# Kernel optimization log

Measured on AMD Instinct MI355X. Metric: run time of the kernel, lower is better.

## Reference

```python
import jax, jax.numpy as jnp
import numpy as np

H = 256; NH = 8; DH = H // NH; L = 2; B = 32; S = 512; FIN = 199; A = 4


def _ln(x, g, b):
    m = jnp.mean(x, -1, keepdims=True)
    v = jnp.mean((x - m) ** 2, -1, keepdims=True)
    return (x - m) / jnp.sqrt(v + 1e-5) * g + b


def _grn(x, fc1w, fc1b, fc2w, fc2b, gw, gb, ggw, ggb, lg, lb):
    # GatedResidualNetwork, input_dim == output_dim so no skip layer, no context
    h = jax.nn.elu(x @ fc1w + fc1b)
    h = jax.nn.elu(h @ fc2w + fc2b)
    g = (h @ gw + gb) * jax.nn.sigmoid(h @ ggw + ggb)  # GLU
    return _ln(g + x, lg, lb)


def _attn(h, wq, bq, wk, bk, wv, bv, wo, bo):
    b, s, _ = h.shape
    q = (h @ wq + bq).reshape(b, s, NH, DH)
    k = (h @ wk + bk).reshape(b, s, NH, DH)
    v = (h @ wv + bv).reshape(b, s, NH, DH)
    scores = jnp.einsum('bqhd,bkhd->bhqk', q, k) / jnp.sqrt(jnp.float32(DH))
    mask = jnp.triu(jnp.ones((s, s), dtype=bool), 1)  # causal: mask strictly-future
    scores = jnp.where(mask, -jnp.inf, scores)
    aw = jax.nn.softmax(scores, axis=-1)
    ctx = jnp.einsum('bhqk,bkhd->bqhd', aw, v).reshape(b, s, H)
    return ctx @ wo + bo, aw


def _pe(s, d):
    pos = jnp.arange(s, dtype=jnp.float32)[:, None]
    div = jnp.exp(jnp.arange(0, d, 2, dtype=jnp.float32) * (-jnp.log(10000.0) / d))
    pe = jnp.zeros((s, d), dtype=jnp.float32)
    pe = pe.at[:, 0::2].set(jnp.sin(pos * div)).at[:, 1::2].set(jnp.cos(pos * div))
    return pe


def setup_inputs():
    key = jax.random.key(0)
    ks = iter(jax.random.split(key, 80))
    def nrm(shape, sc=0.02):
        return (jax.random.normal(next(ks), shape) * sc).astype(jnp.float32)
    d = {}
    d['x'] = jax.random.normal(next(ks), (B, S, FIN), dtype=jnp.float32)
    d['time_features'] = jax.random.normal(next(ks), (B, S, 3), dtype=jnp.float32)
    d['fp_w'] = nrm((FIN, H)); d['fp_b'] = jnp.zeros((H,), jnp.float32)
    d['tp_w'] = nrm((3, H));   d['tp_b'] = jnp.zeros((H,), jnp.float32)
    d['ip_w'] = nrm((H, H));   d['ip_b'] = jnp.zeros((H,), jnp.float32)
    for nm in ['wq', 'wk', 'wv', 'wo']:
        d[nm] = nrm((L, H, H))
    for nm in ['bq', 'bk', 'bv', 'bo']:
        d[nm] = jnp.zeros((L, H), jnp.float32)
    d['ln_g'] = jnp.ones((L, H), jnp.float32); d['ln_b'] = jnp.zeros((L, H), jnp.float32)
    for nm in ['g_fc1w', 'g_fc2w', 'g_gw', 'g_ggw']:
        d[nm] = nrm((L, H, H))
    for nm in ['g_fc1b', 'g_fc2b', 'g_gb', 'g_ggb']:
        d[nm] = jnp.zeros((L, H), jnp.float32)
    d['g_lg'] = jnp.ones((L, H), jnp.float32); d['g_lb'] = jnp.zeros((L, H), jnp.float32)
    for nm in ['f_fc1w', 'f_fc2w', 'f_gw', 'f_ggw']:
        d[nm] = nrm((H, H))
    for nm in ['f_fc1b', 'f_fc2b', 'f_gb', 'f_ggb']:
        d[nm] = jnp.zeros((H,), jnp.float32)
    d['f_lg'] = jnp.ones((H,), jnp.float32); d['f_lb'] = jnp.zeros((H,), jnp.float32)
    d['out_w'] = nrm((H, A)); d['out_b'] = jnp.zeros((A,), jnp.float32)
    return d


def reference(x, time_features, fp_w, fp_b, tp_w, tp_b, ip_w, ip_b,
              wq, bq, wk, bk, wv, bv, wo, bo, ln_g, ln_b,
              g_fc1w, g_fc1b, g_fc2w, g_fc2b, g_gw, g_gb, g_ggw, g_ggb, g_lg, g_lb,
              f_fc1w, f_fc1b, f_fc2w, f_fc2b, f_gw, f_gb, f_ggw, f_ggb, f_lg, f_lb,
              out_w, out_b):
    s = x.shape[1]
    hidden = (x @ fp_w + fp_b) + (time_features @ tp_w + tp_b)
    hidden = hidden @ ip_w + ip_b
    hidden = hidden + _pe(s, H)[None]
    aw = None
    for i in range(L):
        ao, aw = _attn(hidden, wq[i], bq[i], wk[i], bk[i], wv[i], bv[i], wo[i], bo[i])
        hidden = _ln(hidden + ao, ln_g[i], ln_b[i])
        hidden = _grn(hidden, g_fc1w[i], g_fc1b[i], g_fc2w[i], g_fc2b[i],
                      g_gw[i], g_gb[i], g_ggw[i], g_ggb[i], g_lg[i], g_lb[i])
    hidden = _grn(hidden, f_fc1w, f_fc1b, f_fc2w, f_fc2b, f_gw, f_gb, f_ggw, f_ggb, f_lg, f_lb)
    final = hidden[:, -1, :]
    logits = final @ out_w + out_b  # [B, A], one column per target asset
    return (logits, aw)
```

## Files before the change

kernel.cpp:

```cpp
#include <hip/hip_runtime.h>
#include <hip/hip_fp16.h>
#include <math.h>
#include <cstddef>

#define H 256
#define NH 8
#define DH 32
#define LAYERS 2
#define BB 32
#define SS 512
#define FINDIM 199
#define AA 4
#define T_TOK (BB*SS)
#define KIN 224
#define TPB 64

typedef unsigned short u16;
typedef unsigned int u32;
typedef __attribute__((ext_vector_type(8))) short short8;
typedef __attribute__((ext_vector_type(4))) float f4;

__device__ __forceinline__ float b2f(u16 v){
  unsigned u = ((unsigned)v) << 16;
  return __builtin_bit_cast(float, u);
}
__device__ __forceinline__ u16 f2b(float f){
  unsigned u = __builtin_bit_cast(unsigned, f);
  unsigned r = (u + 0x7fffu + ((u >> 16) & 1u)) >> 16;
  return (u16)r;
}
__device__ __forceinline__ float wave_sum(float v){
  #pragma unroll
  for (int mk=1; mk<64; mk<<=1) v += __shfl_xor(v, mk, 64);
  return v;
}

#define GLD_LDS16(g, l) \
  __builtin_amdgcn_global_load_lds((const __attribute__((address_space(1))) void*)(g), \
                                   (__attribute__((address_space(3))) void*)(l), 16, 0, 0)

#define SA (KIN+8)
#define SY (H+8)

template<int KC, int WK>
__device__ __forceinline__ void stage_acc64(
    const u16* Xl, int sx, const u16* __restrict__ Wt,
    int r0, int c0, int l16, int lq, f4 acc[2][4])
{
  #pragma unroll
  for (int mi=0;mi<2;mi++)
    #pragma unroll
    for (int ni=0;ni<4;ni++) acc[mi][ni] = (f4){0.f,0.f,0.f,0.f};
  #pragma unroll
  for (int kc=0;kc<KC;kc++){
    short8 af[2], bf[4];
    #pragma unroll
    for (int mi=0;mi<2;mi++)
      af[mi] = *(const short8*)&Xl[(r0 + mi*16 + l16)*sx + kc*32 + lq*8];
    #pragma unroll
    for (int ni=0;ni<4;ni++)
      bf[ni] = *(const short8*)(Wt + (size_t)(c0 + ni*16 + l16)*WK + kc*32 + lq*8);
    #pragma unroll
    for (int mi=0;mi<2;mi++)
      #pragma unroll
      for (int ni=0;ni<4;ni++)
        acc[mi][ni] = __builtin_amdgcn_mfma_f32_16x16x32_bf16(af[mi], bf[ni], acc[mi][ni], 0,0,0);
  }
}

template<int DO_ELU>
__device__ __forceinline__ void stage_store64(
    f4 acc[2][4], const float* __restrict__ bias,
    int r0, int c0, int l16, int lq, u16* Yl, int sy)
{
  #pragma unroll
  for (int ni=0;ni<4;ni++){
    int col = c0 + ni*16 + l16;
    float bc = bias[col];
    #pragma unroll
    for (int mi=0;mi<2;mi++){
      #pragma unroll
      for (int r=0;r<4;r++){
        int row = r0 + mi*16 + lq*4 + r;
        float v = acc[mi][ni][r] + bc;
        if (DO_ELU) v = v > 0.f ? v : expm1f(v);
        Yl[row*sy + col] = f2b(v);
      }
    }
  }
}

__device__ __forceinline__ void tile_load64(const u16* g, u16* Yl, int sy, int t){
  #pragma unroll
  for (int j=0;j<4;j++){
    int u = t + j*512;
    int row = u >> 5, cu = u & 31;
    *(short8*)&Yl[row*sy + cu*8] = *(const short8*)(g + (size_t)row*H + cu*8);
  }
}

template<int WB>
__device__ __forceinline__ void tile_ln64(
    u16* Yl, int sy, const float* __restrict__ g, const float* __restrict__ b,
    u16* out, int t)
{
  int w = t >> 6, lane = t & 63;
  #pragma unroll
  for (int rr=0;rr<8;rr++){
    int row = w*8 + rr;
    float xv[4];
    #pragma unroll
    for (int j=0;j<4;j++) xv[j] = b2f(Yl[row*sy + lane*4 + j]);
    float s=0.f, ss=0.f;
    #pragma unroll
    for (int j=0;j<4;j++){ s += xv[j]; ss += xv[j]*xv[j]; }
    s = wave_sum(s); ss = wave_sum(ss);
    float mean = s * (1.0f/H);
    float var  = ss * (1.0f/H) - mean*mean;
    float rstd = rsqrtf(var + 1e-5f);
    ushort4 o;
    int col = lane*4;
    o.x = f2b((xv[0]-mean)*rstd*g[col+0] + b[col+0]);
    o.y = f2b((xv[1]-mean)*rstd*g[col+1] + b[col+1]);
    o.z = f2b((xv[2]-mean)*rstd*g[col+2] + b[col+2]);
    o.w = f2b((xv[3]-mean)*rstd*g[col+3] + b[col+3]);
    *(ushort4*)(out + (size_t)row*H + col) = o;
    if (WB && row == 63) *(ushort4*)(Yl + row*sy + col) = o;
  }
}

struct WPtrs { const float* p[21]; };

__global__ __launch_bounds__(256) void wconv_kernel(WPtrs wp, u16* __restrict__ dst){
  __shared__ float tl[64][65];
  int mb = blockIdx.x >> 4, tile = blockIdx.x & 15;
  int k0 = (tile >> 2) * 64, n0 = (tile & 3) * 64;
  const float* src = wp.p[mb];
  int t = threadIdx.x;
  int r = t >> 4, cg = t & 15;
  #pragma unroll
  for (int p4=0;p4<4;p4++){
    f4 v = *(const f4*)(src + (size_t)(k0 + r + p4*16)*H + n0 + cg*4);
    tl[r+p4*16][cg*4+0]=v[0]; tl[r+p4*16][cg*4+1]=v[1];
    tl[r+p4*16][cg*4+2]=v[2]; tl[r+p4*16][cg*4+3]=v[3];
  }
  __syncthreads();
  u16* db = dst + (size_t)mb*H*H;
  #pragma unroll
  for (int p4=0;p4<4;p4++){
    int rn = r + p4*16;
    ushort4 o;
    o.x = f2b(tl[cg*4+0][rn]); o.y = f2b(tl[cg*4+1][rn]);
    o.z = f2b(tl[cg*4+2][rn]); o.w = f2b(tl[cg*4+3][rn]);
    *(ushort4*)(db + (size_t)(n0+rn)*H + k0 + cg*4) = o;
  }
}

__global__ __launch_bounds__(256) void wcat_kernel(
    const float* __restrict__ fp_w, const float* __restrict__ tp_w,
    u16* __restrict__ wcat){
  int idx = blockIdx.x*256 + threadIdx.x;
  if (idx >= 256*KIN) return;
  int n = idx / KIN, k2 = idx % KIN;
  float v = 0.f;
  if (k2 < FINDIM) v = fp_w[(size_t)k2*H + n];
  else if (k2 < FINDIM+3) v = tp_w[(size_t)(k2-FINDIM)*H + n];
  wcat[idx] = f2b(v);
}

__global__ __launch_bounds__(256) void xconv_kernel(
    const float* __restrict__ x, const float* __restrict__ tf,
    u16* __restrict__ ab){
  size_t idx = (size_t)blockIdx.x*256 + threadIdx.x;
  if (idx >= (size_t)T_TOK*KIN) return;
  int tok = idx / KIN, k2 = idx % KIN;
  float v = 0.f;
  if (k2 < FINDIM) v = x[(size_t)tok*FINDIM + k2];
  else if (k2 < FINDIM+3) v = tf[(size_t)tok*3 + (k2-FINDIM)];
  ab[idx] = f2b(v);
}

__global__ __launch_bounds__(512,4) void input_kernel(
    const u16* __restrict__ ab, const u16* __restrict__ wcat,
    const float* __restrict__ fp_b, const float* __restrict__ tp_b,
    const u16* __restrict__ ipw, const float* __restrict__ ip_b,
    u16* __restrict__ hid){
  __shared__ u16 Al[TPB*SA];
  __shared__ u16 Tl[TPB*SY];
  int t = threadIdx.x;
  int tok0 = blockIdx.x * TPB;
  int lane = t & 63, w = t >> 6;
  int l16 = lane & 15, lq = lane >> 4;
  int r0 = (w >> 2) * 32;
  int c0 = (w & 3) * 64;

  #pragma unroll
  for (int j=0;j<4;j++){
    int u = t + j*512;
    if (u < 1792){
      int row = u / 28, cu = u % 28;
      *(short8*)&Al[row*SA + cu*8] = *(const short8*)(ab + (size_t)(tok0+row)*KIN + cu*8);
    }
  }
  __syncthreads();

  f4 acc[2][4];
  stage_acc64<7, KIN>(Al, SA, wcat, r0, c0, l16, lq, acc);
  #pragma unroll
  for (int ni=0;ni<4;ni++){
    int col = c0 + ni*16 + l16;
    float bc = fp_b[col] + tp_b[col];
    #pragma unroll
    for (int mi=0;mi<2;mi++)
      #pragma unroll
      for (int r=0;r<4;r++){
        int row = r0 + mi*16 + lq*4 + r;
        Tl[row*SY + col] = f2b(acc[mi][ni][r] + bc);
      }
  }
  __syncthreads();

  stage_acc64<8, H>(Tl, SY, ipw, r0, c0, l16, lq, acc);
  #pragma unroll
  for (int ni=0;ni<4;ni++){
    int col = c0 + ni*16 + l16;
    float bc = ip_b[col];
    int ii = col >> 1;
    float div = __expf((float)(2*ii) * -0.03597789207803197f);
    #pragma unroll
    for (int mi=0;mi<2;mi++)
      #pragma unroll
      for (int r=0;r<4;r++){
        int row = r0 + mi*16 + lq*4 + r;
        int s = (tok0 + row) & (SS-1);
        float arg = (float)s * div;
        float pe = (col & 1) ? cosf(arg) : sinf(arg);
        hid[(size_t)(tok0+row)*H + col] = f2b(acc[mi][ni][r] + bc + pe);
      }
  }
}

__global__ __launch_bounds__(512,4) void oproj_ln_kernel(
    const u16* __restrict__ ctx, u16* __restrict__ hid,
    const u16* __restrict__ wo, const float* __restrict__ bo,
    const float* __restrict__ g, const float* __restrict__ b){
  __shared__ u16 Xl[TPB*SY];
  int t = threadIdx.x;
  int tok0 = blockIdx.x * TPB;
  int lane = t & 63, w = t >> 6;
  int l16 = lane & 15, lq = lane >> 4;
  int r0 = (w >> 2) * 32;
  int c0 = (w & 3) * 64;
  u16* hb = hid + (size_t)tok0*H;

  tile_load64(ctx + (size_t)tok0*H, Xl, SY, t);
  __syncthreads();

  f4 acc[2][4];
  stage_acc64<8, H>(Xl, SY, wo, r0, c0, l16, lq, acc);
  __syncthreads();
  #pragma unroll
  for (int ni=0;ni<4;ni++){
    int col = c0 + ni*16 + l16;
    float bc = bo[col];
    #pragma unroll
    for (int mi=0;mi<2;mi++)
      #pragma unroll
      for (int r=0;r<4;r++){
        int row = r0 + mi*16 + lq*4 + r;
        float y = acc[mi][ni][r] + bc + b2f(hb[(size_t)row*H + col]);
        Xl[row*SY + col] = f2b(y);
      }
  }
  __syncthreads();
  tile_ln64<0>(Xl, SY, g, b, hb, t);
}

template<int LOGITS>
__global__ __launch_bounds__(512,4) void grn_kernel(
    u16* __restrict__ hid,
    const u16* __restrict__ fc1, const u16* __restrict__ fc2,
    const u16* __restrict__ gw,  const u16* __restrict__ ggw,
    const float* __restrict__ b1, const float* __restrict__ b2,
    const float* __restrict__ gb, const float* __restrict__ ggb,
    const float* __restrict__ lg, const float* __restrict__ lb,
    const float* __restrict__ ow, const float* __restrict__ ob,
    float* __restrict__ lout){
  __shared__ u16 Xa[TPB*SY];
  __shared__ u16 Xb[TPB*SY];
  int t = threadIdx.x;
  int tok0 = blockIdx.x * TPB;
  int lane = t & 63, w = t >> 6;
  int l16 = lane & 15, lq = lane >> 4;
  int r0 = (w >> 2) * 32;
  int c0 = (w & 3) * 64;
  u16* hb = hid + (size_t)tok0*H;

  tile_load64(hb, Xa, SY, t);
  __syncthreads();

  f4 acc[2][4];
  stage_acc64<8, H>(Xa, SY, fc1, r0, c0, l16, lq, acc);
  stage_store64<1>(acc, b1, r0, c0, l16, lq, Xb, SY);
  __syncthreads();
  stage_acc64<8, H>(Xb, SY, fc2, r0, c0, l16, lq, acc);
  stage_store64<1>(acc, b2, r0, c0, l16, lq, Xa, SY);
  __syncthreads();

  stage_acc64<8, H>(Xa, SY, ggw, r0, c0, l16, lq, acc);
  u32 sgp[2][4][2];
  #pragma unroll
  for (int mi=0;mi<2;mi++)
    #pragma unroll
    for (int ni=0;ni<4;ni++){
      float bc = ggb[c0 + ni*16 + l16];
      float s0 = 1.0f/(1.0f + __expf(-(acc[mi][ni][0]+bc)));
      float s1 = 1.0f/(1.0f + __expf(-(acc[mi][ni][1]+bc)));
      float s2 = 1.0f/(1.0f + __expf(-(acc[mi][ni][2]+bc)));
      float s3 = 1.0f/(1.0f + __expf(-(acc[mi][ni][3]+bc)));
      sgp[mi][ni][0] = __builtin_bit_cast(u32, __floats2half2_rn(s0, s1));
      sgp[mi][ni][1] = __builtin_bit_cast(u32, __floats2half2_rn(s2, s3));
    }

  stage_acc64<8, H>(Xa, SY, gw, r0, c0, l16, lq, acc);
  #pragma unroll
  for (int ni=0;ni<4;ni++){
    int col = c0 + ni*16 + l16;
    float bc = gb[col];
    #pragma unroll
    for (int mi=0;mi<2;mi++){
      float2 s01 = __half22float2(__builtin_bit_cast(__half2, sgp[mi][ni][0]));
      float2 s23 = __half22float2(__builtin_bit_cast(__half2, sgp[mi][ni][1]));
      float sv[4] = {s01.x, s01.y, s23.x, s23.y};
      #pragma unroll
      for (int r=0;r<4;r++){
        int row = r0 + mi*16 + lq*4 + r;
        float y = (acc[mi][ni][r] + bc) * sv[r] + b2f(hb[(size_t)row*H + col]);
        Xb[row*SY + col] = f2b(y);
      }
    }
  }
  __syncthreads();
  tile_ln64<LOGITS>(Xb, SY, lg, lb, hb, t);

  if (LOGITS){
    if ((tok0 & (SS-1)) == SS - TPB){
      __syncthreads();
      if (t < 64){
        int bidx = tok0 >> 9;
        float a0=0.f, a1=0.f, a2=0.f, a3=0.f;
        #pragma unroll
        for (int j=0;j<4;j++){
          int k = t*4 + j;
          float xv = b2f(Xb[63*SY + k]);
          f4 wr = *(const f4*)(ow + (size_t)k*AA);
          a0 = fmaf(xv, wr[0], a0);
          a1 = fmaf(xv, wr[1], a1);
          a2 = fmaf(xv, wr[2], a2);
          a3 = fmaf(xv, wr[3], a3);
        }
        a0 = wave_sum(a0); a1 = wave_sum(a1);
        a2 = wave_sum(a2); a3 = wave_sum(a3);
        if (t == 0){
          lout[bidx*AA+0] = a0 + ob[0];
          lout[bidx*AA+1] = a1 + ob[1];
          lout[bidx*AA+2] = a2 + ob[2];
          lout[bidx*AA+3] = a3 + ob[3];
        }
      }
    }
  }
}

struct GemmJob  { const u16* Wt; const float* bias; u16* C; };
struct GemmBatch{ GemmJob j[3]; };

__global__ __launch_bounds__(256) void gemm_bf16(
    const u16* __restrict__ A, GemmBatch jb) {
  __shared__ u16 smem[128*64 + 64*64];
  u16* As  = smem;
  u16* Wsm = smem + 128*64;
  const GemmJob job = jb.j[blockIdx.z];
  const u16* Wt = job.Wt;
  int t = threadIdx.x;
  int m0 = blockIdx.x * 128;
  int n0 = blockIdx.y * 64;
  int lane = t & 63, w = t >> 6;
  int wr = (w >> 1) * 64;
  int wc = (w & 1) * 32;
  int l16 = lane & 15, lq = lane >> 4;

  f4 acc[4][2];
  #pragma unroll
  for (int mi=0;mi<4;mi++)
    #pragma unroll
    for (int ni=0;ni<2;ni++) acc[mi][ni] = (f4){0.f,0.f,0.f,0.f};

  for (int k0=0;k0<256;k0+=64){
    #pragma unroll
    for (int ja=0;ja<4;ja++){
      int ub = (w*4 + ja)*64;
      int u  = ub + lane;
      int m  = u >> 3, c = u & 7, kx = c ^ (m & 7);
      const u16* g = A + (size_t)(m0+m)*H + k0 + kx*8;
      GLD_LDS16(g, As + (size_t)ub*8);
    }
    #pragma unroll
    for (int jb2=0;jb2<2;jb2++){
      int ub = (w*2 + jb2)*64;
      int u  = ub + lane;
      int n  = u >> 3, c = u & 7, kx = c ^ (n & 7);
      const u16* g = Wt + (size_t)(n0+n)*H + k0 + kx*8;
      GLD_LDS16(g, Wsm + (size_t)ub*8);
    }
    __syncthreads();
    #pragma unroll
    for (int kc=0;kc<2;kc++){
      short8 af[4], bf[2];
      int kx = kc*4 + lq;
      #pragma unroll
      for (int mi=0;mi<4;mi++){
        int m = wr + mi*16 + l16;
        int un = (m<<3) | (kx ^ (m&7));
        af[mi] = *(short8*)&As[un*8];
      }
      #pragma unroll
      for (int ni=0;ni<2;ni++){
        int n = wc + ni*16 + l16;
        int un = (n<<3) | (kx ^ (n&7));
        bf[ni] = *(short8*)&Wsm[un*8];
      }
      #pragma unroll
      for (int mi=0;mi<4;mi++)
        #pragma unroll
        for (int ni=0;ni<2;ni++)
          acc[mi][ni] = __builtin_amdgcn_mfma_f32_16x16x32_bf16(af[mi], bf[ni], acc[mi][ni], 0,0,0);
    }
    __syncthreads();
  }

  u16* Cl = smem;
  #pragma unroll
  for (int ni=0;ni<2;ni++){
    int coll = wc + ni*16 + l16;
    float bcol = job.bias[n0 + coll];
    #pragma unroll
    for (int mi=0;mi<4;mi++){
      #pragma unroll
      for (int r=0;r<4;r++){
        int rowl = wr + mi*16 + lq*4 + r;
        Cl[rowl*68 + coll] = f2b(acc[mi][ni][r] + bcol);
      }
    }
  }
  __syncthreads();
  #pragma unroll
  for (int q2=0;q2<4;q2++){
    int u = q2*256 + t;
    int row = u >> 3, cu = u & 7;
    short8 val = *(short8*)&Cl[row*68 + cu*8];
    *(short8*)(job.C + (size_t)(m0+row)*H + n0 + cu*8) = val;
  }
}

template<int WRITE_AW>
__global__ __launch_bounds__(256) void attn_kernel(
    const u16* __restrict__ q, const u16* __restrict__ k,
    const u16* __restrict__ v, float* __restrict__ aw,
    u16* __restrict__ ctx) {
  __shared__ u16 Vt[DH][SS+8];
  __shared__ u16 Plds[4][16][72];
  int t  = threadIdx.x;
  int zg = blockIdx.x;
  int bh = blockIdx.y;
  int b  = bh >> 3, h = bh & 7;
  int lane = t & 63, w = t >> 6;
  int l16 = lane & 15, lq = lane >> 4;
  const float scale = 0.17677669529663687f;

  #pragma unroll
  for (int rep=0;rep<2;rep++){
    int kk = t + rep*256;
    const u16* vp = v + ((size_t)(b*SS + kk))*H + h*DH;
    short8 r0 = *(const short8*)(vp);
    short8 r1 = *(const short8*)(vp+8);
    short8 r2 = *(const short8*)(vp+16);
    short8 r3 = *(const short8*)(vp+24);
    #pragma unroll
    for (int j=0;j<8;j++){
      Vt[j][kk]    = (u16)r0[j];
      Vt[8+j][kk]  = (u16)r1[j];
      Vt[16+j][kk] = (u16)r2[j];
      Vt[24+j][kk] = (u16)r3[j];
    }
  }
  __syncthreads();

  for (int it=0; it<4; it++){
    int qt  = zg + it*2;
    int qr0 = qt*64 + w*16;
    int KT  = qt*4 + w + 1;
    short8 af = *(const short8*)(q + ((size_t)(b*SS + qr0 + l16))*H + h*DH + lq*8);

    float l[4] = {0.f,0.f,0.f,0.f};
    f4 o[2] = {(f4){0.f,0.f,0.f,0.f}, (f4){0.f,0.f,0.f,0.f}};
    u32 pk0[32], pk1[32];

    #pragma unroll
    for (int c8=0;c8<8;c8++){
      if (c8*4 < KT){
        #pragma unroll
        for (int j=0;j<4;j++){
          int kt = c8*4 + j;
          float p[4] = {0.f,0.f,0.f,0.f};
          if (kt < KT){
            short8 bfr = *(const short8*)(k + ((size_t)(b*SS + kt*16 + l16))*H + h*DH + lq*8);
            f4 cc = (f4){0.f,0.f,0.f,0.f};
            cc = __builtin_amdgcn_mfma_f32_16x16x32_bf16(af, bfr, cc, 0,0,0);
            int col = kt*16 + l16;
            #pragma unroll
            for (int i=0;i<4;i++){
              int qi = qr0 + lq*4 + i;
              float sc = (col <= qi) ? cc[i]*scale : -3.0e38f;
              p[i] = __expf(sc);
              l[i] += p[i];
            }
          }
          u16 pb[4];
          #pragma unroll
          for (int i=0;i<4;i++) pb[i] = f2b(p[i]);
          if (WRITE_AW){
            pk0[kt] = (u32)pb[0] | ((u32)pb[1] << 16);
            pk1[kt] = (u32)pb[2] | ((u32)pb[3] << 16);
          }
          #pragma unroll
          for (int i=0;i<4;i++) Plds[w][lq*4+i][j*16+l16] = pb[i];
        }
        #pragma unroll
        for (int kc=0;kc<2;kc++){
          short8 pa = *(short8*)&Plds[w][l16][kc*32 + lq*8];
          #pragma unroll
          for (int dt=0;dt<2;dt++){
            short8 vb = *(const short8*)&Vt[dt*16 + l16][c8*64 + kc*32 + lq*8];
            o[dt] = __builtin_amdgcn_mfma_f32_16x16x32_bf16(pa, vb, o[dt], 0,0,0);
          }
        }
      }
    }

    #pragma unroll
    for (int i=0;i<4;i++){
      #pragma unroll
      for (int mk=1; mk<16; mk<<=1) l[i] += __shfl_xor(l[i], mk, 64);
    }
    float inv[4];
    #pragma unroll
    for (int i=0;i<4;i++) inv[i] = 1.0f / l[i];

    if (WRITE_AW){
      float* ab = aw + (size_t)bh*SS*SS;
      #pragma unroll
      for (int kt=0;kt<32;kt++){
        if (kt < KT){
          int col = kt*16 + l16;
          float pv[4] = { b2f((u16)pk0[kt]), b2f((u16)(pk0[kt]>>16)),
                          b2f((u16)pk1[kt]), b2f((u16)(pk1[kt]>>16)) };
          #pragma unroll
          for (int i=0;i<4;i++){
            int qi = qr0 + lq*4 + i;
            float val = (col <= qi) ? pv[i]*inv[i] : 0.f;
            __builtin_nontemporal_store(val, &ab[(size_t)qi*SS + col]);
          }
        }
      }
      int c4base = KT*4;
      f4 z = (f4){0.f,0.f,0.f,0.f};
      #pragma unroll
      for (int ri=0;ri<4;ri++){
        int row = qr0 + ri*4 + lq;
        for (int j=l16; j < 128 - c4base; j += 16)
          __builtin_nontemporal_store(z, (f4*)&ab[(size_t)row*SS + (size_t)(c4base+j)*4]);
      }
    }

    #pragma unroll
    for (int dt=0;dt<2;dt++){
      #pragma unroll
      for (int i=0;i<4;i++){
        int row = qr0 + lq*4 + i;
        ctx[((size_t)(b*SS + row))*H + h*DH + dt*16 + l16] = f2b(o[dt][i]*inv[i]);
      }
    }
  }
}

extern "C" void kernel_launch(void* const* d_in, const int* in_sizes, int n_in,
                              void* d_out, int out_size, void* d_ws, size_t ws_size,
                              hipStream_t stream){
  (void)in_sizes; (void)n_in; (void)out_size; (void)ws_size;
  const float* x      = (const float*)d_in[0];
  const float* tf     = (const float*)d_in[1];
  const float* fp_w   = (const float*)d_in[2];
  const float* fp_b   = (const float*)d_in[3];
  const float* tp_w   = (const float*)d_in[4];
  const float* tp_b   = (const float*)d_in[5];
  const float* ip_w   = (const float*)d_in[6];
  const float* ip_b   = (const float*)d_in[7];
  const float* wq     = (const float*)d_in[8];
  const float* wk     = (const float*)d_in[9];
  const float* wv     = (const float*)d_in[10];
  const float* wo     = (const float*)d_in[11];
  const float* bq     = (const float*)d_in[12];
  const float* bk     = (const float*)d_in[13];
  const float* bv     = (const float*)d_in[14];
  const float* bo     = (const float*)d_in[15];
  const float* ln_g   = (const float*)d_in[16];
  const float* ln_b   = (const float*)d_in[17];
  const float* g_fc1w = (const float*)d_in[18];
  const float* g_fc2w = (const float*)d_in[19];
  const float* g_gw   = (const float*)d_in[20];
  const float* g_ggw  = (const float*)d_in[21];
  const float* g_fc1b = (const float*)d_in[22];
  const float* g_fc2b = (const float*)d_in[23];
  const float* g_gb   = (const float*)d_in[24];
  const float* g_ggb  = (const float*)d_in[25];
  const float* g_lg   = (const float*)d_in[26];
  const float* g_lb   = (const float*)d_in[27];
  const float* f_fc1w = (const float*)d_in[28];
  const float* f_fc2w = (const float*)d_in[29];
  const float* f_gw   = (const float*)d_in[30];
  const float* f_ggw  = (const float*)d_in[31];
  const float* f_fc1b = (const float*)d_in[32];
  const float* f_fc2b = (const float*)d_in[33];
  const float* f_gb   = (const float*)d_in[34];
  const float* f_ggb  = (const float*)d_in[35];
  const float* f_lg   = (const float*)d_in[36];
  const float* f_lb   = (const float*)d_in[37];
  const float* out_w  = (const float*)d_in[38];
  const float* out_b  = (const float*)d_in[39];

  float* logits = (float*)d_out;
  float* aw     = logits + BB*AA;

  u16* wts = (u16*)d_ws;
  const size_t WMAT = (size_t)H*H;
  u16* wcat = wts  + 21*WMAT;
  u16* abuf = wcat + (size_t)H*KIN;
  u16* hid  = abuf + (size_t)T_TOK*KIN;
  size_t BUF = (size_t)T_TOK * H;
  u16* buf1 = hid  + BUF;
  u16* buf2 = buf1 + BUF;
  u16* buf3 = buf2 + BUF;

  WPtrs wp;
  wp.p[0]  = ip_w;
  wp.p[1]  = wq;        wp.p[2]  = wq + WMAT;
  wp.p[3]  = wk;        wp.p[4]  = wk + WMAT;
  wp.p[5]  = wv;        wp.p[6]  = wv + WMAT;
  wp.p[7]  = wo;        wp.p[8]  = wo + WMAT;
  wp.p[9]  = g_fc1w;    wp.p[10] = g_fc1w + WMAT;
  wp.p[11] = g_fc2w;    wp.p[12] = g_fc2w + WMAT;
  wp.p[13] = g_gw;      wp.p[14] = g_gw + WMAT;
  wp.p[15] = g_ggw;     wp.p[16] = g_ggw + WMAT;
  wp.p[17] = f_fc1w;    wp.p[18] = f_fc2w;
  wp.p[19] = f_gw;      wp.p[20] = f_ggw;
  const int WT_IP=0, WT_Q=1, WT_K=3, WT_V=5, WT_O=7,
            WT_FC1=9, WT_FC2=11, WT_GW=13, WT_GGW=15,
            WT_FFC1=17, WT_FFC2=18, WT_FGW=19, WT_FGGW=20;

  dim3 b256(256), b512(512);
  dim3 gAttn(2, BB*NH);
  dim3 gTok(T_TOK/TPB);

  wconv_kernel<<<21*16, b256, 0, stream>>>(wp, wts);
  wcat_kernel<<<(H*KIN+255)/256, b256, 0, stream>>>(fp_w, tp_w, wcat);
  xconv_kernel<<<(T_TOK*KIN+255)/256, b256, 0, stream>>>(x, tf, abuf);
  input_kernel<<<gTok, b512, 0, stream>>>(abuf, wcat, fp_b, tp_b,
                                          wts + (size_t)WT_IP*WMAT, ip_b, hid);

  for (int i=0;i<LAYERS;i++){
    const size_t BOFF = (size_t)i*H;
    GemmBatch gb;
    gb.j[0] = { wts + (size_t)(WT_Q+i)*WMAT, bq+BOFF, buf1 };
    gb.j[1] = { wts + (size_t)(WT_K+i)*WMAT, bk+BOFF, buf2 };
    gb.j[2] = { wts + (size_t)(WT_V+i)*WMAT, bv+BOFF, buf3 };
    gemm_bf16<<<dim3(T_TOK/128, H/64, 3), b256, 0, stream>>>(hid, gb);
    if (i == LAYERS-1)
      attn_kernel<1><<<gAttn, b256, 0, stream>>>(buf1, buf2, buf3, aw, buf1);
    else
      attn_kernel<0><<<gAttn, b256, 0, stream>>>(buf1, buf2, buf3, aw, buf1);
    oproj_ln_kernel<<<gTok, b512, 0, stream>>>(buf1, hid,
        wts + (size_t)(WT_O+i)*WMAT, bo+BOFF, ln_g+BOFF, ln_b+BOFF);
    grn_kernel<0><<<gTok, b512, 0, stream>>>(hid,
        wts + (size_t)(WT_FC1+i)*WMAT, wts + (size_t)(WT_FC2+i)*WMAT,
        wts + (size_t)(WT_GW+i)*WMAT,  wts + (size_t)(WT_GGW+i)*WMAT,
        g_fc1b+BOFF, g_fc2b+BOFF, g_gb+BOFF, g_ggb+BOFF,
        g_lg+BOFF, g_lb+BOFF, nullptr, nullptr, nullptr);
  }

  grn_kernel<1><<<gTok, b512, 0, stream>>>(hid,
      wts + (size_t)WT_FFC1*WMAT, wts + (size_t)WT_FFC2*WMAT,
      wts + (size_t)WT_FGW*WMAT,  wts + (size_t)WT_FGGW*WMAT,
      f_fc1b, f_fc2b, f_gb, f_ggb, f_lg, f_lb,
      out_w, out_b, logits);
}
```

Before: 688.3 us.

## Split attention into one block per query tile and stage residuals in LDS

The attention grid grows from 2 to 8 blocks per (batch, head). Each block now handles a single 64-row query tile and loads only the causal prefix of V into LDS, instead of looping over four tiles with the full V staged. The oproj and GRN kernels now stage the residual tile in shared memory rather than re-reading it from global memory with strided accesses, which adds LDS use and extra barriers. Launch-bound occupancy hints drop from 4 to 2 blocks per CU, which gives the compiler more registers but may reduce latency hiding.

Result: no change. 678.6 us (-1.4%).

```diff
diff --git a/kernel.cpp b/kernel.cpp
--- a/kernel.cpp
+++ b/kernel.cpp
@@ -180,7 +180,7 @@
   ab[idx] = f2b(v);
 }
 
-__global__ __launch_bounds__(512,4) void input_kernel(
+__global__ __launch_bounds__(512,2) void input_kernel(
     const u16* __restrict__ ab, const u16* __restrict__ wcat,
     const float* __restrict__ fp_b, const float* __restrict__ tp_b,
     const u16* __restrict__ ipw, const float* __restrict__ ip_b,
@@ -240,11 +240,12 @@
   }
 }
 
-__global__ __launch_bounds__(512,4) void oproj_ln_kernel(
+__global__ __launch_bounds__(512,2) void oproj_ln_kernel(
     const u16* __restrict__ ctx, u16* __restrict__ hid,
     const u16* __restrict__ wo, const float* __restrict__ bo,
     const float* __restrict__ g, const float* __restrict__ b){
   __shared__ u16 Xl[TPB*SY];
+  __shared__ u16 Rl[TPB*SY];
   int t = threadIdx.x;
   int tok0 = blockIdx.x * TPB;
   int lane = t & 63, w = t >> 6;
@@ -254,6 +255,7 @@
   u16* hb = hid + (size_t)tok0*H;
 
   tile_load64(ctx + (size_t)tok0*H, Xl, SY, t);
+  tile_load64(hb, Rl, SY, t);
   __syncthreads();
 
   f4 acc[2][4];
@@ -268,7 +270,7 @@
       #pragma unroll
       for (int r=0;r<4;r++){
         int row = r0 + mi*16 + lq*4 + r;
-        float y = acc[mi][ni][r] + bc + b2f(hb[(size_t)row*H + col]);
+        float y = acc[mi][ni][r] + bc + b2f(Rl[row*SY + col]);
         Xl[row*SY + col] = f2b(y);
       }
   }
@@ -277,7 +279,7 @@
 }
 
 template<int LOGITS>
-__global__ __launch_bounds__(512,4) void grn_kernel(
+__global__ __launch_bounds__(512,2) void grn_kernel(
     u16* __restrict__ hid,
     const u16* __restrict__ fc1, const u16* __restrict__ fc2,
     const u16* __restrict__ gw,  const u16* __restrict__ ggw,
@@ -304,10 +306,11 @@
   stage_store64<1>(acc, b1, r0, c0, l16, lq, Xb, SY);
   __syncthreads();
   stage_acc64<8, H>(Xb, SY, fc2, r0, c0, l16, lq, acc);
-  stage_store64<1>(acc, b2, r0, c0, l16, lq, Xa, SY);
-  __syncthreads();
-
-  stage_acc64<8, H>(Xa, SY, ggw, r0, c0, l16, lq, acc);
+  __syncthreads();
+  stage_store64<1>(acc, b2, r0, c0, l16, lq, Xb, SY);
+  __syncthreads();
+
+  stage_acc64<8, H>(Xb, SY, ggw, r0, c0, l16, lq, acc);
   u32 sgp[2][4][2];
   #pragma unroll
   for (int mi=0;mi<2;mi++)
@@ -322,7 +325,8 @@
       sgp[mi][ni][1] = __builtin_bit_cast(u32, __floats2half2_rn(s2, s3));
     }
 
-  stage_acc64<8, H>(Xa, SY, gw, r0, c0, l16, lq, acc);
+  stage_acc64<8, H>(Xb, SY, gw, r0, c0, l16, lq, acc);
+  __syncthreads();
   #pragma unroll
   for (int ni=0;ni<4;ni++){
     int col = c0 + ni*16 + l16;
@@ -335,7 +339,7 @@
       #pragma unroll
       for (int r=0;r<4;r++){
         int row = r0 + mi*16 + lq*4 + r;
-        float y = (acc[mi][ni][r] + bc) * sv[r] + b2f(hb[(size_t)row*H + col]);
+        float y = (acc[mi][ni][r] + bc) * sv[r] + b2f(Xa[row*SY + col]);
         Xb[row*SY + col] = f2b(y);
       }
     }
@@ -471,33 +475,31 @@
   __shared__ u16 Vt[DH][SS+8];
   __shared__ u16 Plds[4][16][72];
   int t  = threadIdx.x;
-  int zg = blockIdx.x;
+  int qt = blockIdx.x;
   int bh = blockIdx.y;
   int b  = bh >> 3, h = bh & 7;
   int lane = t & 63, w = t >> 6;
   int l16 = lane & 15, lq = lane >> 4;
   const float scale = 0.17677669529663687f;
 
-  #pragma unroll
-  for (int rep=0;rep<2;rep++){
-    int kk = t + rep*256;
+  int nrows = (qt+1)*64;
+  for (int kk = t; kk < nrows; kk += 256){
     const u16* vp = v + ((size_t)(b*SS + kk))*H + h*DH;
-    short8 r0 = *(const short8*)(vp);
-    short8 r1 = *(const short8*)(vp+8);
-    short8 r2 = *(const short8*)(vp+16);
-    short8 r3 = *(const short8*)(vp+24);
+    short8 r0v = *(const short8*)(vp);
+    short8 r1v = *(const short8*)(vp+8);
+    short8 r2v = *(const short8*)(vp+16);
+    short8 r3v = *(const short8*)(vp+24);
     #pragma unroll
     for (int j=0;j<8;j++){
-      Vt[j][kk]    = (u16)r0[j];
-      Vt[8+j][kk]  = (u16)r1[j];
-      Vt[16+j][kk] = (u16)r2[j];
-      Vt[24+j][kk] = (u16)r3[j];
-    }
-  }
-  __syncthreads();
-
-  for (int it=0; it<4; it++){
-    int qt  = zg + it*2;
+      Vt[j][kk]    = (u16)r0v[j];
+      Vt[8+j][kk]  = (u16)r1v[j];
+      Vt[16+j][kk] = (u16)r2v[j];
+      Vt[24+j][kk] = (u16)r3v[j];
+    }
+  }
+  __syncthreads();
+
+  {
     int qr0 = qt*64 + w*16;
     int KT  = qt*4 + w + 1;
     short8 af = *(const short8*)(q + ((size_t)(b*SS + qr0 + l16))*H + h*DH + lq*8);
@@ -669,7 +671,7 @@
             WT_FFC1=17, WT_FFC2=18, WT_FGW=19, WT_FGGW=20;
 
   dim3 b256(256), b512(512);
-  dim3 gAttn(2, BB*NH);
+  dim3 gAttn(8, BB*NH);
   dim3 gTok(T_TOK/TPB);
 
   wconv_kernel<<<21*16, b256, 0, stream>>>(wp, wts);
```
